# Performance work log

Measured on AMD Instinct MI355X. Metric: run time of the kernel, lower is better.

## Reference

```python
import jax, jax.numpy as jnp
import numpy as np

N_NODES = 100000
N_EDGES = 1600000
D_IN = 128
D_OUT = 128


def setup_inputs() -> dict:
    key = jax.random.key(0)
    k_x, k_e, k_wl, k_bl, k_wr = jax.random.split(key, 5)
    x = jax.random.normal(k_x, (N_NODES, D_IN), dtype=jnp.float32)
    edge_index = jax.random.randint(k_e, (2, N_EDGES), 0, N_NODES, dtype=jnp.int64)
    # PyG Linear default init ~ kaiming-uniform-ish; plain uniform is fine for a numeric reference
    s = 1.0 / np.sqrt(D_IN)
    W_l = jax.random.uniform(k_wl, (D_OUT, D_IN), minval=-s, maxval=s, dtype=jnp.float32)
    b_l = jax.random.uniform(k_bl, (D_OUT,), minval=-s, maxval=s, dtype=jnp.float32)
    W_r = jax.random.uniform(k_wr, (D_OUT, D_IN), minval=-s, maxval=s, dtype=jnp.float32)
    return {"x": x, "edge_index": edge_index, "W_l": W_l, "b_l": b_l, "W_r": W_r}


def reference(x, edge_index, W_l, b_l, W_r):
    # SAGEConv (mean aggr): messages flow src -> dst
    src = edge_index[0]  # [E]
    dst = edge_index[1]  # [E]
    msgs = x[src]  # [E, D_IN] neighbor gather
    summed = jax.ops.segment_sum(msgs, dst, num_segments=N_NODES)  # [N, D_IN]
    deg = jax.ops.segment_sum(jnp.ones_like(dst, dtype=x.dtype), dst, num_segments=N_NODES)  # [N]
    agg = summed / jnp.maximum(deg, 1.0)[:, None]  # mean with 0 for isolated nodes
    # out = lin_l(agg) + lin_r(x); bias only on lin_l (PyG default)
    out = agg @ W_l.T + b_l + x @ W_r.T
    return out
```

## Files before the change

kernel.cpp:

```cpp
#include <hip/hip_runtime.h>

#define D_FEAT 128
#define CAP 32
#define S1CAP (1 << 16)
#define S2CAP (1 << 16)
#define LOGB 7
#define LOCB 128
#define BCAP 2560
#define CHUNK 16384
#define NBUK_MAX 1024

typedef short bf16x8 __attribute__((ext_vector_type(8)));
typedef float f32x4 __attribute__((ext_vector_type(4)));

__device__ __forceinline__ unsigned short f2bf(float f) {
    unsigned u = __builtin_bit_cast(unsigned, f);
    u += 0x7FFF + ((u >> 16) & 1);
    return (unsigned short)(u >> 16);
}


__global__ __launch_bounds__(256) void prep_kernel(
    const int* __restrict__ ei, int* __restrict__ flag, int* __restrict__ s1cnt,
    int* __restrict__ s2cnt, int* __restrict__ bincnt, int NBUK,
    const float* __restrict__ Wl, const float* __restrict__ Wr,
    unsigned short* __restrict__ Wc,
    const float4* __restrict__ x4, uint2* __restrict__ xb2, long total4) {
    const int b = blockIdx.x;
    const int t = threadIdx.x;
    if (b == 0) {
        __shared__ int nzs[4];
        int nz = 0;
        for (int i = t; i < 4096; i += 256) nz |= (ei[2 * i + 1] != 0);
        unsigned long long bal = __ballot(nz);
        if ((t & 63) == 0) nzs[t >> 6] = (bal != 0ull) ? 1 : 0;
        __syncthreads();
        if (t == 0) {
            *flag = (nzs[0] | nzs[1] | nzs[2] | nzs[3]) ? 0 : 1;
            *s1cnt = 0;
            *s2cnt = 0;
        }
        for (int i = t; i < NBUK; i += 256) bincnt[i] = 0;
    } else if (b <= 128) {
        int n = b - 1;
        float w = (t < 128) ? Wl[n * 128 + t] : Wr[n * 128 + (t - 128)];
        Wc[n * 256 + t] = f2bf(w);
    } else {
        long gid = (long)(b - 129) * 256 + t;
        if (gid < total4) {
            float4 v = x4[gid];
            uint2 o;
            o.x = (unsigned)f2bf(v.x) | ((unsigned)f2bf(v.y) << 16);
            o.y = (unsigned)f2bf(v.z) | ((unsigned)f2bf(v.w) << 16);
            xb2[gid] = o;
        }
    }
}

__global__ __launch_bounds__(256) void bin_kernel(
    const int* __restrict__ ei, const int* __restrict__ flag,
    int* __restrict__ bincnt, unsigned* __restrict__ bins,
    int* __restrict__ s1cnt, int* __restrict__ spill1, int E, int N, int NBUK) {
    __shared__ int hist[NBUK_MAX];
    __shared__ int rbase[NBUK_MAX];
    const int t = threadIdx.x;
    const long e0 = (long)blockIdx.x * CHUNK;
    const int cnt = (int)min((long)CHUNK, (long)E - e0);
    const int is64 = *flag;

    for (int i = t; i < NBUK; i += 256) hist[i] = 0;
    __syncthreads();

    for (int i = t; i < cnt; i += 256) {
        long e = e0 + i;
        int dst = is64 ? (int)((const long long*)ei)[(long)E + e] : ei[(long)E + e];
        dst = min(max(dst, 0), N - 1);
        atomicAdd(&hist[dst >> LOGB], 1);
    }
    __syncthreads();

    for (int i = t; i < NBUK; i += 256) {
        int h = hist[i];
        rbase[i] = (h > 0) ? atomicAdd(&bincnt[i], h) : 0;
        hist[i] = 0;
    }
    __syncthreads();

    for (int i = t; i < cnt; i += 256) {
        long e = e0 + i;
        int src, dst;
        if (is64) {
            src = (int)((const long long*)ei)[e];
            dst = (int)((const long long*)ei)[(long)E + e];
        } else {
            src = ei[e];
            dst = ei[(long)E + e];
        }
        src = min(max(src, 0), N - 1);
        dst = min(max(dst, 0), N - 1);
        int bk = dst >> LOGB;
        int slot = rbase[bk] + atomicAdd(&hist[bk], 1);
        if (slot < BCAP) {
            bins[(long)bk * BCAP + slot] = ((unsigned)(dst & (LOCB - 1)) << 25) | (unsigned)src;
        } else {
            int sp = atomicAdd(s1cnt, 1);
            if (sp < S1CAP) {
                spill1[2 * sp] = src;
                spill1[2 * sp + 1] = dst;
            }
        }
    }
}

__global__ __launch_bounds__(256) void fill2_kernel(
    const unsigned* __restrict__ bins, const int* __restrict__ bincnt,
    int* __restrict__ adj, int* __restrict__ cursor,
    int* __restrict__ s2cnt, int* __restrict__ spill2, int N) {
    __shared__ int cur[LOCB];
    const int bk = blockIdx.x;
    const int t = threadIdx.x;
    if (t < LOCB) cur[t] = 0;
    __syncthreads();
    const int cnt = min(bincnt[bk], BCAP);
    const int nb = bk << LOGB;
    for (int i = t; i < cnt; i += 256) {
        unsigned v = bins[(long)bk * BCAP + i];
        int src = (int)(v & 0x1FFFFFFu);
        int ld = (int)(v >> 25);
        int slot = atomicAdd(&cur[ld], 1);
        int dst = nb + ld;
        if (slot < CAP) {
            adj[(long)dst * CAP + slot] = src;
        } else {
            int sp = atomicAdd(s2cnt, 1);
            if (sp < S2CAP) {
                spill2[2 * sp] = src;
                spill2[2 * sp + 1] = dst;
            }
        }
    }
    __syncthreads();
    if (t < LOCB && nb + t < N) cursor[nb + t] = cur[t];
}

__global__ __launch_bounds__(256) void spillfill_kernel(
    const int* __restrict__ s1cnt, const int* __restrict__ spill1,
    int* __restrict__ cursor, int* __restrict__ adj,
    int* __restrict__ s2cnt, int* __restrict__ spill2) {
    const int sc = min(*s1cnt, S1CAP);
    for (int i = blockIdx.x * 256 + threadIdx.x; i < sc; i += gridDim.x * 256) {
        int src = spill1[2 * i];
        int dst = spill1[2 * i + 1];
        int slot = atomicAdd(&cursor[dst], 1);
        if (slot < CAP) {
            adj[(long)dst * CAP + slot] = src;
        } else {
            int sp = atomicAdd(s2cnt, 1);
            if (sp < S2CAP) {
                spill2[2 * sp] = src;
                spill2[2 * sp + 1] = dst;
            }
        }
    }
}

__device__ __forceinline__ void acc_row(float* acc, uint4 v) {
    acc[0] += __builtin_bit_cast(float, v.x << 16);
    acc[1] += __builtin_bit_cast(float, v.x & 0xFFFF0000u);
    acc[2] += __builtin_bit_cast(float, v.y << 16);
    acc[3] += __builtin_bit_cast(float, v.y & 0xFFFF0000u);
    acc[4] += __builtin_bit_cast(float, v.z << 16);
    acc[5] += __builtin_bit_cast(float, v.z & 0xFFFF0000u);
    acc[6] += __builtin_bit_cast(float, v.w << 16);
    acc[7] += __builtin_bit_cast(float, v.w & 0xFFFF0000u);
}

__device__ __forceinline__ int pick_src(int adjv, int adjv2, int e, int cq, int qd) {
    int ec = e & 31;
    int s = __shfl((ec < 16) ? adjv : adjv2, qd * 16 + (ec & 15));
    return (e < cq) ? s : 0;
}

__global__ __launch_bounds__(256) void gg_kernel(
    const unsigned int* __restrict__ xb, const int* __restrict__ cursor,
    const int* __restrict__ adj, const unsigned short* __restrict__ Wc,
    const float* __restrict__ bl, float* __restrict__ out, int N) {
    __shared__ __align__(16) unsigned short A[16 * 264];

    const int t = threadIdx.x;
    const int wv = t >> 6;
    const int lane = t & 63;
    const int n0 = blockIdx.x * 16;
    const int fq = lane & 15;
    const int qd = lane >> 4;

    const int n = n0 + wv * 4 + qd;
    const int nc = min(n, N - 1);

    const int deg = (n < N) ? cursor[n] : 0;
    int adjv = adj[(long)nc * CAP + fq];
    int adjv2 = adj[(long)nc * CAP + 16 + fq];

    unsigned xv[4];
#pragma unroll
    for (int q = 0; q < 4; ++q) {
        int nn = n0 + wv * 4 + q;
        xv[q] = (nn < N) ? xb[(long)nn * 64 + lane] : 0u;
    }

    adjv = min(max(adjv, 0), N - 1);
    adjv2 = min(max(adjv2, 0), N - 1);

    const int cq = min(deg, CAP);
    int mx = max(cq, __shfl_xor(cq, 16));
    mx = max(mx, __shfl_xor(mx, 32));
    mx = (mx + 3) & ~3;

    float acc[8] = {0.f, 0.f, 0.f, 0.f, 0.f, 0.f, 0.f, 0.f};
    uint4 va[4], vb[4];
#pragma unroll
    for (int j = 0; j < 4; ++j) {
        int s = pick_src(adjv, adjv2, j, cq, qd);
        va[j] = *(const uint4*)&xb[(long)s * 64 + fq * 4];
    }
    for (int base = 0; base < mx; base += 4) {
#pragma unroll
        for (int j = 0; j < 4; ++j) {
            int s = pick_src(adjv, adjv2, base + 4 + j, cq, qd);
            vb[j] = *(const uint4*)&xb[(long)s * 64 + fq * 4];
        }
#pragma unroll
        for (int j = 0; j < 4; ++j) {
            if (base + j < cq) acc_row(acc, va[j]);
        }
#pragma unroll
        for (int j = 0; j < 4; ++j) va[j] = vb[j];
    }

    const float iv = 1.0f / (float)max(deg, 1);
    uint4 o;
    o.x = (unsigned)f2bf(acc[0] * iv) | ((unsigned)f2bf(acc[1] * iv) << 16);
    o.y = (unsigned)f2bf(acc[2] * iv) | ((unsigned)f2bf(acc[3] * iv) << 16);
    o.z = (unsigned)f2bf(acc[4] * iv) | ((unsigned)f2bf(acc[5] * iv) << 16);
    o.w = (unsigned)f2bf(acc[6] * iv) | ((unsigned)f2bf(acc[7] * iv) << 16);
    *(uint4*)&A[(wv * 4 + qd) * 264 + fq * 8] = o;
#pragma unroll
    for (int q = 0; q < 4; ++q)
        *(unsigned*)&A[(wv * 4 + q) * 264 + 128 + 2 * lane] = xv[q];
    __syncthreads();

    const int l15 = lane & 15;
    const int quad = lane >> 4;
    f32x4 acc2[2];
    acc2[0] = (f32x4){0.f, 0.f, 0.f, 0.f};
    acc2[1] = (f32x4){0.f, 0.f, 0.f, 0.f};

#pragma unroll
    for (int kc = 0; kc < 8; ++kc) {
        const int k0 = kc * 32;
        bf16x8 af = *(const bf16x8*)&A[l15 * 264 + k0 + quad * 8];
#pragma unroll
        for (int nt = 0; nt < 2; ++nt) {
            int col = wv * 32 + nt * 16 + l15;
            bf16x8 bf = *(const bf16x8*)&Wc[col * 256 + k0 + quad * 8];
            acc2[nt] = __builtin_amdgcn_mfma_f32_16x16x32_bf16(af, bf, acc2[nt], 0, 0, 0);
        }
    }

#pragma unroll
    for (int nt = 0; nt < 2; ++nt) {
        int col = wv * 32 + nt * 16 + l15;
        float bias = bl[col];
#pragma unroll
        for (int r = 0; r < 4; ++r) {
            int node = n0 + quad * 4 + r;
            if (node < N) out[(long)node * 128 + col] = acc2[nt][r] + bias;
        }
    }
}

__global__ __launch_bounds__(256) void spill2_kernel(
    const float* __restrict__ x, const float* __restrict__ Wl,
    const int* __restrict__ cursor, const int* __restrict__ s2cnt,
    const int* __restrict__ spill2, float* __restrict__ out) {
    const int wv = threadIdx.x >> 6;
    const int lane = threadIdx.x & 63;
    const int sc = min(*s2cnt, S2CAP);
    for (int i = blockIdx.x * 4 + wv; i < sc; i += gridDim.x * 4) {
        int src = spill2[2 * i];
        int dst = spill2[2 * i + 1];
        float inv = 1.0f / (float)max(cursor[dst], 1);
#pragma unroll
        for (int cc = 0; cc < 2; ++cc) {
            int c = lane + cc * 64;
            float s = 0.0f;
            for (int k = 0; k < 128; k += 4) {
                float4 w4 = *(const float4*)&Wl[c * 128 + k];
                float4 x4 = *(const float4*)&x[(long)src * 128 + k];
                s += w4.x * x4.x + w4.y * x4.y + w4.z * x4.z + w4.w * x4.w;
            }
            atomicAdd(&out[(long)dst * 128 + c], s * inv);
        }
    }
}

extern "C" void kernel_launch(void* const* d_in, const int* in_sizes, int n_in,
                              void* d_out, int out_size, void* d_ws, size_t ws_size,
                              hipStream_t stream) {
    const float* x = (const float*)d_in[0];
    const int* ei = (const int*)d_in[1];
    const float* Wl = (const float*)d_in[2];
    const float* bl = (const float*)d_in[3];
    const float* Wr = (const float*)d_in[4];
    float* out = (float*)d_out;

    const int N = in_sizes[0] / D_FEAT;
    const int E = in_sizes[1] / 2;
    const int NBUK = (N + LOCB - 1) >> LOGB;

    int* wsI = (int*)d_ws;
    int* flag = wsI;
    int* cursor = flag + 64;
    int* s1cnt = cursor + N;
    int* spill1 = s1cnt + 64;
    int* s2cnt = spill1 + 2 * S1CAP;
    int* spill2 = s2cnt + 64;
    int* bincnt = spill2 + 2 * S2CAP;
    unsigned* bins = (unsigned*)(bincnt + NBUK_MAX);
    int* adj = (int*)(bins + (long)NBUK * BCAP);
    unsigned short* Wc = (unsigned short*)(adj + (long)N * CAP);
    unsigned int* xb = (unsigned int*)(Wc + 128 * 256);

    const long total4 = (long)N * 32;
    const int XBB = (int)((total4 + 255) / 256);

    prep_kernel<<<1 + 128 + XBB, 256, 0, stream>>>(ei, flag, s1cnt, s2cnt, bincnt,
                                                   NBUK, Wl, Wr, Wc,
                                                   (const float4*)x, (uint2*)xb, total4);
    bin_kernel<<<(E + CHUNK - 1) / CHUNK, 256, 0, stream>>>(ei, flag, bincnt, bins,
                                                            s1cnt, spill1, E, N, NBUK);
    fill2_kernel<<<NBUK, 256, 0, stream>>>(bins, bincnt, adj, cursor, s2cnt, spill2, N);
    spillfill_kernel<<<64, 256, 0, stream>>>(s1cnt, spill1, cursor, adj, s2cnt, spill2);
    gg_kernel<<<(N + 15) / 16, 256, 0, stream>>>(xb, cursor, adj, Wc, bl, out, N);
    spill2_kernel<<<64, 256, 0, stream>>>(x, Wl, cursor, s2cnt, spill2, out);
}
```

Baseline: 290.3 us.

## Fuse edge binning with weight/x conversion and fold spill fill into fill2

```diff
diff --git a/kernel.cpp b/kernel.cpp
--- a/kernel.cpp
+++ b/kernel.cpp
@@ -7,8 +7,9 @@
 #define LOGB 7
 #define LOCB 128
 #define BCAP 2560
-#define CHUNK 16384
+#define CHUNK 8192
 #define NBUK_MAX 1024
+#define BPAD 8
 
 typedef short bf16x8 __attribute__((ext_vector_type(8)));
 typedef float f32x4 __attribute__((ext_vector_type(4)));
@@ -20,14 +21,12 @@
 }
 
 
-__global__ __launch_bounds__(256) void prep_kernel(
+__global__ __launch_bounds__(256) void tprep_kernel(
     const int* __restrict__ ei, int* __restrict__ flag, int* __restrict__ s1cnt,
-    int* __restrict__ s2cnt, int* __restrict__ bincnt, int NBUK,
-    const float* __restrict__ Wl, const float* __restrict__ Wr,
-    unsigned short* __restrict__ Wc,
-    const float4* __restrict__ x4, uint2* __restrict__ xb2, long total4) {
+    int* __restrict__ s2cnt, int* __restrict__ bincnt) {
     const int b = blockIdx.x;
     const int t = threadIdx.x;
+    for (int i = b * 256 + t; i < NBUK_MAX * BPAD; i += 8 * 256) bincnt[i] = 0;
     if (b == 0) {
         __shared__ int nzs[4];
         int nz = 0;
@@ -40,13 +39,76 @@
             *s1cnt = 0;
             *s2cnt = 0;
         }
-        for (int i = t; i < NBUK; i += 256) bincnt[i] = 0;
-    } else if (b <= 128) {
-        int n = b - 1;
+    }
+}
+
+__global__ __launch_bounds__(256) void bwx_kernel(
+    const int* __restrict__ ei, const int* __restrict__ flag,
+    int* __restrict__ bincnt, unsigned* __restrict__ bins,
+    int* __restrict__ s1cnt, int* __restrict__ spill1, int E, int N, int NBUK,
+    int BINB,
+    const float* __restrict__ Wl, const float* __restrict__ Wr,
+    unsigned short* __restrict__ Wc,
+    const float4* __restrict__ x4, uint2* __restrict__ xb2, long total4) {
+    const int b = blockIdx.x;
+    const int t = threadIdx.x;
+
+    if (b < BINB) {
+        __shared__ int hist[NBUK_MAX];
+        __shared__ int rbase[NBUK_MAX];
+        const long e0 = (long)b * CHUNK;
+        const int cnt = (int)min((long)CHUNK, (long)E - e0);
+        const int is64 = *flag;
+
+        for (int i = t; i < NBUK; i += 256) hist[i] = 0;
+        __syncthreads();
+
+        for (int i = t; i < cnt; i += 256) {
+            long e = e0 + i;
+            int dst = is64 ? (int)((const long long*)ei)[(long)E + e] : ei[(long)E + e];
+            dst = min(max(dst, 0), N - 1);
+            atomicAdd(&hist[dst >> LOGB], 1);
+        }
+        __syncthreads();
+
+        for (int i = t; i < NBUK; i += 256) {
+            int h = hist[i];
+            rbase[i] = (h > 0) ? atomicAdd(&bincnt[i * BPAD], h) : 0;
+            hist[i] = 0;
+        }
+        __syncthreads();
+
+        for (int i = t; i < cnt; i += 256) {
+            long e = e0 + i;
+            int src, dst;
+            if (is64) {
+                src = (int)((const long long*)ei)[e];
+                dst = (int)((const long long*)ei)[(long)E + e];
+            } else {
+                src = ei[e];
+                dst = ei[(long)E + e];
+            }
+            src = min(max(src, 0), N - 1);
+            dst = min(max(dst, 0), N - 1);
+            int bk = dst >> LOGB;
+            int slot = rbase[bk] + atomicAdd(&hist[bk], 1);
+            if (slot < BCAP) {
+                bins[(long)bk * BCAP + slot] =
+                    ((unsigned)(dst & (LOCB - 1)) << 25) | (unsigned)src;
+            } else {
+                int sp = atomicAdd(s1cnt, 1);
+                if (sp < S1CAP) {
+                    spill1[2 * sp] = src;
+                    spill1[2 * sp + 1] = dst;
+                }
+            }
+        }
+    } else if (b < BINB + 128) {
+        int n = b - BINB;
         float w = (t < 128) ? Wl[n * 128 + t] : Wr[n * 128 + (t - 128)];
         Wc[n * 256 + t] = f2bf(w);
     } else {
-        long gid = (long)(b - 129) * 256 + t;
+        long gid = (long)(b - BINB - 128) * 256 + t;
         if (gid < total4) {
             float4 v = x4[gid];
             uint2 o;
@@ -57,71 +119,17 @@
     }
 }
 
-__global__ __launch_bounds__(256) void bin_kernel(
-    const int* __restrict__ ei, const int* __restrict__ flag,
-    int* __restrict__ bincnt, unsigned* __restrict__ bins,
-    int* __restrict__ s1cnt, int* __restrict__ spill1, int E, int N, int NBUK) {
-    __shared__ int hist[NBUK_MAX];
-    __shared__ int rbase[NBUK_MAX];
-    const int t = threadIdx.x;
-    const long e0 = (long)blockIdx.x * CHUNK;
-    const int cnt = (int)min((long)CHUNK, (long)E - e0);
-    const int is64 = *flag;
-
-    for (int i = t; i < NBUK; i += 256) hist[i] = 0;
-    __syncthreads();
-
-    for (int i = t; i < cnt; i += 256) {
-        long e = e0 + i;
-        int dst = is64 ? (int)((const long long*)ei)[(long)E + e] : ei[(long)E + e];
-        dst = min(max(dst, 0), N - 1);
-        atomicAdd(&hist[dst >> LOGB], 1);
-    }
-    __syncthreads();
-
-    for (int i = t; i < NBUK; i += 256) {
-        int h = hist[i];
-        rbase[i] = (h > 0) ? atomicAdd(&bincnt[i], h) : 0;
-        hist[i] = 0;
-    }
-    __syncthreads();
-
-    for (int i = t; i < cnt; i += 256) {
-        long e = e0 + i;
-        int src, dst;
-        if (is64) {
-            src = (int)((const long long*)ei)[e];
-            dst = (int)((const long long*)ei)[(long)E + e];
-        } else {
-            src = ei[e];
-            dst = ei[(long)E + e];
-        }
-        src = min(max(src, 0), N - 1);
-        dst = min(max(dst, 0), N - 1);
-        int bk = dst >> LOGB;
-        int slot = rbase[bk] + atomicAdd(&hist[bk], 1);
-        if (slot < BCAP) {
-            bins[(long)bk * BCAP + slot] = ((unsigned)(dst & (LOCB - 1)) << 25) | (unsigned)src;
-        } else {
-            int sp = atomicAdd(s1cnt, 1);
-            if (sp < S1CAP) {
-                spill1[2 * sp] = src;
-                spill1[2 * sp + 1] = dst;
-            }
-        }
-    }
-}
-
 __global__ __launch_bounds__(256) void fill2_kernel(
     const unsigned* __restrict__ bins, const int* __restrict__ bincnt,
     int* __restrict__ adj, int* __restrict__ cursor,
+    const int* __restrict__ s1cnt, const int* __restrict__ spill1,
     int* __restrict__ s2cnt, int* __restrict__ spill2, int N) {
     __shared__ int cur[LOCB];
     const int bk = blockIdx.x;
     const int t = threadIdx.x;
     if (t < LOCB) cur[t] = 0;
     __syncthreads();
-    const int cnt = min(bincnt[bk], BCAP);
+    const int cnt = min(bincnt[bk * BPAD], BCAP);
     const int nb = bk << LOGB;
     for (int i = t; i < cnt; i += 256) {
         unsigned v = bins[(long)bk * BCAP + i];
@@ -139,29 +147,26 @@
             }
         }
     }
+    const int sc = min(*s1cnt, S1CAP);
+    for (int i = t; i < sc; i += 256) {
+        int dst = spill1[2 * i + 1];
+        if ((dst >> LOGB) == bk) {
+            int src = spill1[2 * i];
+            int ld = dst & (LOCB - 1);
+            int slot = atomicAdd(&cur[ld], 1);
+            if (slot < CAP) {
+                adj[(long)dst * CAP + slot] = src;
+            } else {
+                int sp = atomicAdd(s2cnt, 1);
+                if (sp < S2CAP) {
+                    spill2[2 * sp] = src;
+                    spill2[2 * sp + 1] = dst;
+                }
+            }
+        }
+    }
     __syncthreads();
     if (t < LOCB && nb + t < N) cursor[nb + t] = cur[t];
-}
-
-__global__ __launch_bounds__(256) void spillfill_kernel(
-    const int* __restrict__ s1cnt, const int* __restrict__ spill1,
-    int* __restrict__ cursor, int* __restrict__ adj,
-    int* __restrict__ s2cnt, int* __restrict__ spill2) {
-    const int sc = min(*s1cnt, S1CAP);
-    for (int i = blockIdx.x * 256 + threadIdx.x; i < sc; i += gridDim.x * 256) {
-        int src = spill1[2 * i];
-        int dst = spill1[2 * i + 1];
-        int slot = atomicAdd(&cursor[dst], 1);
-        if (slot < CAP) {
-            adj[(long)dst * CAP + slot] = src;
-        } else {
-            int sp = atomicAdd(s2cnt, 1);
-            if (sp < S2CAP) {
-                spill2[2 * sp] = src;
-                spill2[2 * sp + 1] = dst;
-            }
-        }
-    }
 }
 
 __device__ __forceinline__ void acc_row(float* acc, uint4 v) {
@@ -317,6 +322,7 @@
     const int N = in_sizes[0] / D_FEAT;
     const int E = in_sizes[1] / 2;
     const int NBUK = (N + LOCB - 1) >> LOGB;
+    const int BINB = (E + CHUNK - 1) / CHUNK;
 
     int* wsI = (int*)d_ws;
     int* flag = wsI;
@@ -326,7 +332,7 @@
     int* s2cnt = spill1 + 2 * S1CAP;
     int* spill2 = s2cnt + 64;
     int* bincnt = spill2 + 2 * S2CAP;
-    unsigned* bins = (unsigned*)(bincnt + NBUK_MAX);
+    unsigned* bins = (unsigned*)(bincnt + NBUK_MAX * BPAD);
     int* adj = (int*)(bins + (long)NBUK * BCAP);
     unsigned short* Wc = (unsigned short*)(adj + (long)N * CAP);
     unsigned int* xb = (unsigned int*)(Wc + 128 * 256);
@@ -334,13 +340,12 @@
     const long total4 = (long)N * 32;
     const int XBB = (int)((total4 + 255) / 256);
 
-    prep_kernel<<<1 + 128 + XBB, 256, 0, stream>>>(ei, flag, s1cnt, s2cnt, bincnt,
-                                                   NBUK, Wl, Wr, Wc,
-                                                   (const float4*)x, (uint2*)xb, total4);
-    bin_kernel<<<(E + CHUNK - 1) / CHUNK, 256, 0, stream>>>(ei, flag, bincnt, bins,
-                                                            s1cnt, spill1, E, N, NBUK);
-    fill2_kernel<<<NBUK, 256, 0, stream>>>(bins, bincnt, adj, cursor, s2cnt, spill2, N);
-    spillfill_kernel<<<64, 256, 0, stream>>>(s1cnt, spill1, cursor, adj, s2cnt, spill2);
+    tprep_kernel<<<8, 256, 0, stream>>>(ei, flag, s1cnt, s2cnt, bincnt);
+    bwx_kernel<<<BINB + 128 + XBB, 256, 0, stream>>>(
+        ei, flag, bincnt, bins, s1cnt, spill1, E, N, NBUK, BINB, Wl, Wr, Wc,
+        (const float4*)x, (uint2*)xb, total4);
+    fill2_kernel<<<NBUK, 256, 0, stream>>>(bins, bincnt, adj, cursor, s1cnt, spill1,
+                                           s2cnt, spill2, N);
     gg_kernel<<<(N + 15) / 16, 256, 0, stream>>>(xb, cursor, adj, Wc, bl, out, N);
     spill2_kernel<<<64, 256, 0, stream>>>(x, Wl, cursor, s2cnt, spill2, out);
 }
```

Measured after the change: 261.4 us. 9.9% less time.
